# Kernel optimization log

Hardware: AMD Instinct MI355X
Metric: run time of the kernel (lower is better)

## Reference

```python
import jax, jax.numpy as jnp
import numpy as np

S_LEN, BATCH, HID, HEADS = 2048, 4, 1024, 16
HD = HID // HEADS


def setup_inputs() -> dict:
    key = jax.random.key(0)
    ks = jax.random.split(key, 6)

    def lin_w(k, out_dim, in_dim):
        return jax.random.normal(k, (out_dim, in_dim), jnp.float32) * (1.0 / np.sqrt(in_dim))

    return {
        "hidden_states": jax.random.normal(ks[0], (S_LEN, BATCH, HID), jnp.float32),
        "Wq": lin_w(ks[1], HID, HID), "bq": jnp.zeros((HID,), jnp.float32),
        "Wk": lin_w(ks[2], HID, HID), "bk": jnp.zeros((HID,), jnp.float32),
        "Wv": lin_w(ks[3], HID, HID), "bv": jnp.zeros((HID,), jnp.float32),
        "Wf": lin_w(ks[4], HEADS, HID), "bf": jnp.zeros((HEADS,), jnp.float32),
        "Wo": lin_w(ks[5], HID, HID), "bo": jnp.zeros((HID,), jnp.float32),
    }


def _forget_attention(hidden_states, Wq, bq, Wk, bk, Wv, bv, Wf, bf, Wo, bo):
    S, B, H = hidden_states.shape
    nh, hd = HEADS, HD

    def shape(x):
        return x.reshape(S, B, nh, hd)

    q = shape(hidden_states @ Wq.T + bq)
    k = shape(hidden_states @ Wk.T + bk)
    v = shape(hidden_states @ Wv.T + bv)

    # kernel_fn = elu(x) + 1
    phi_q = jax.nn.elu(q) + 1.0
    phi_k = jax.nn.elu(k) + 1.0

    f = jax.nn.sigmoid(hidden_states @ Wf.T + bf)  # [S, B, nh]

    # F_{t,j} = prod_{i=j+1}^{t} f_i  factorizes into the recurrence:
    #   S_t = f_t * S_{t-1} + phi_k_t (x) v_t ;  z_t = f_t * z_{t-1} + phi_k_t
    # out_t = (phi_q_t . S_t) / (phi_q_t . z_t + eps)
    def step(carry, xs):
        Sm, z = carry                      # [B,nh,hd,hd], [B,nh,hd]
        ft, pk, pq, vt = xs                # [B,nh], [B,nh,hd] x3
        fte = ft[..., None]
        Sm = fte[..., None] * Sm + pk[..., :, None] * vt[..., None, :]
        z = fte * z + pk
        num = jnp.einsum('bhd,bhde->bhe', pq, Sm)
        den = jnp.einsum('bhd,bhd->bh', pq, z)[..., None]
        return (Sm, z), num / (den + 1e-6)

    init = (jnp.zeros((B, nh, hd, hd), hidden_states.dtype),
            jnp.zeros((B, nh, hd), hidden_states.dtype))
    _, out = jax.lax.scan(step, init, (f, phi_k, phi_q, v))

    out = out.reshape(S, B, H) @ Wo.T + bo
    return out, f


def reference(hidden_states, Wq, bq, Wk, bk, Wv, bv, Wf, bf, Wo, bo):
    out, f = _forget_attention(hidden_states, Wq, bq, Wk, bk, Wv, bv, Wf, bf, Wo, bo)
    return (out, jnp.zeros_like(out), f)
```

## Files before the change

### kernel.cpp

```cpp
#include <hip/hip_runtime.h>
#include <hip/hip_bf16.h>
#include <math.h>

#define S_LEN 2048
#define BATCH 4
#define HID   1024
#define HEADS 16
#define HD    64
#define SB    (S_LEN*BATCH)
#define CHUNK 64
#define NCHUNK (S_LEN/CHUNK)
#define BH    (BATCH*HEADS)
#define NSTK  3200

typedef __bf16 bf16x8 __attribute__((ext_vector_type(8)));
typedef float  f32x4  __attribute__((ext_vector_type(4)));
typedef unsigned short ushort_t;
typedef unsigned short u16x8 __attribute__((ext_vector_type(8)));
typedef unsigned short u16x4 __attribute__((ext_vector_type(4)));

__device__ __forceinline__ unsigned short f2bf(float x) {
    union { float f; unsigned int u; } un; un.f = x;
    unsigned int u = un.u;
    unsigned int r = (u + 0x7FFFu + ((u >> 16) & 1u)) >> 16;
    return (unsigned short)r;
}
__device__ __forceinline__ float bf2f(unsigned short s) {
    union { unsigned int u; float f; } un; un.u = ((unsigned int)s) << 16;
    return un.f;
}

#define GLL16(src, dst) __builtin_amdgcn_global_load_lds( \
    (const __attribute__((address_space(1))) void*)(src), \
    (__attribute__((address_space(3))) void*)(dst), 16, 0, 0)

#define NXU (SB*HID/4)
#define NW1 (NSTK*HID/4)
#define NW2 (HID*HID/4)
#define NBU (NSTK/4)
#define NTOT (NXU+NW1+NW2+NBU)

__global__ __launch_bounds__(256) void prep_kernel(
    const float* __restrict__ X,  const float* __restrict__ Wq,
    const float* __restrict__ Wk, const float* __restrict__ Wv,
    const float* __restrict__ Wf, const float* __restrict__ Wo,
    const float* __restrict__ bq, const float* __restrict__ bk,
    const float* __restrict__ bv, const float* __restrict__ bf,
    ushort_t* __restrict__ Xb, ushort_t* __restrict__ Wstk,
    ushort_t* __restrict__ Wob, float* __restrict__ bstk)
{
    const int i = blockIdx.x * 256 + threadIdx.x;
    if (i < NXU) {
        float4 v = ((const float4*)X)[i];
        ushort4 o; o.x=f2bf(v.x); o.y=f2bf(v.y); o.z=f2bf(v.z); o.w=f2bf(v.w);
        ((ushort4*)Xb)[i] = o;
    } else if (i < NXU + NW1) {
        const int idx4 = (i - NXU) * 4;
        const int row = idx4 >> 10, col = idx4 & 1023;
        float4 v;
        if      (row < 1024) v = *(const float4*)(Wq + (size_t)row*HID + col);
        else if (row < 2048) v = *(const float4*)(Wk + (size_t)(row-1024)*HID + col);
        else if (row < 3072) v = *(const float4*)(Wv + (size_t)(row-2048)*HID + col);
        else if (row < 3088) v = *(const float4*)(Wf + (size_t)(row-3072)*HID + col);
        else                 v = make_float4(0.f,0.f,0.f,0.f);
        ushort4 o; o.x=f2bf(v.x); o.y=f2bf(v.y); o.z=f2bf(v.z); o.w=f2bf(v.w);
        *(ushort4*)(Wstk + idx4) = o;
    } else if (i < NXU + NW1 + NW2) {
        const int idx4 = (i - NXU - NW1) * 4;
        float4 v = *(const float4*)(Wo + idx4);
        ushort4 o; o.x=f2bf(v.x); o.y=f2bf(v.y); o.z=f2bf(v.z); o.w=f2bf(v.w);
        *(ushort4*)(Wob + idx4) = o;
    } else if (i < NTOT) {
        const int idx4 = (i - NXU - NW1 - NW2) * 4;
        #pragma unroll
        for (int t = 0; t < 4; ++t) {
            const int c = idx4 + t;
            float v;
            if      (c < 1024) v = bq[c];
            else if (c < 2048) v = bk[c-1024];
            else if (c < 3072) v = bv[c-2048];
            else if (c < 3088) v = bf[c-3072];
            else               v = 0.f;
            bstk[c] = v;
        }
    }
}

__global__ __launch_bounds__(256) void qkvf_gemm(
    const ushort_t* __restrict__ X, const ushort_t* __restrict__ W,
    const float* __restrict__ bias,
    ushort_t* __restrict__ Q, ushort_t* __restrict__ Kr,
    ushort_t* __restrict__ V,
    float* __restrict__ f_out, float* __restrict__ logf_out)
{
    __shared__ ushort_t As[128 * 32];
    __shared__ ushort_t Bs[128 * 32];

    const int tid  = threadIdx.x;
    const int wave = tid >> 6, lane = tid & 63;
    const int waveM = wave >> 1, waveN = wave & 1;

    const int lin = blockIdx.y * 64 + blockIdx.x;
    const int L   = (lin & 7) * 200 + (lin >> 3);
    const int rowBase = (L & 63) * 128;
    const int colBase = (L >> 6) * 128;
    const int K = HID;

    f32x4 acc[4][4];
    #pragma unroll
    for (int i = 0; i < 4; ++i)
        #pragma unroll
        for (int j = 0; j < 4; ++j)
            acc[i][j] = (f32x4){0.f, 0.f, 0.f, 0.f};

    const int srow = lane >> 2;
    const int scol = (lane & 3) * 8;

    const ushort_t* gA0 = X + (size_t)(rowBase + wave*16 + srow) * K + scol;
    const ushort_t* gB0 = W + (size_t)(colBase + wave*16 + srow) * K + scol;
    ushort_t* lA = As + (wave*16)*32;
    ushort_t* lB = Bs + (wave*16)*32;

    const int fr = lane & 15;
    const int fk = (lane >> 4) * 8;

    for (int k0 = 0; k0 < K; k0 += 32) {
        GLL16(gA0 + k0,                lA);
        GLL16(gA0 + (size_t)64*K + k0, lA + 64*32);
        GLL16(gB0 + k0,                lB);
        GLL16(gB0 + (size_t)64*K + k0, lB + 64*32);

        __syncthreads();

        bf16x8 a[4], b[4];
        #pragma unroll
        for (int i = 0; i < 4; ++i)
            a[i] = *(const bf16x8*)(As + (waveM*64 + i*16 + fr)*32 + fk);
        #pragma unroll
        for (int j = 0; j < 4; ++j)
            b[j] = *(const bf16x8*)(Bs + (waveN*64 + j*16 + fr)*32 + fk);

        #pragma unroll
        for (int i = 0; i < 4; ++i)
            #pragma unroll
            for (int j = 0; j < 4; ++j)
                acc[i][j] = __builtin_amdgcn_mfma_f32_16x16x32_bf16(
                    a[i], b[j], acc[i][j], 0, 0, 0);

        __syncthreads();
    }

    const int er = (lane >> 4) * 4;
    const int ec = lane & 15;
    #pragma unroll
    for (int i = 0; i < 4; ++i) {
        #pragma unroll
        for (int j = 0; j < 4; ++j) {
            const int r0 = rowBase + waveM*64 + i*16 + er;
            const int c0 = colBase + waveN*64 + j*16;
            if (c0 >= 3088) continue;
            const int c  = c0 + ec;
            const float bv = bias[c];
            #pragma unroll
            for (int k = 0; k < 4; ++k) {
                float v = acc[i][j][k] + bv;
                const int r = r0 + k;
                if (c0 < 1024) {
                    v = (v > 0.f) ? (v + 1.f) : __expf(v);
                    Q[(size_t)r * HID + c] = f2bf(v);
                } else if (c0 < 2048) {
                    v = (v > 0.f) ? (v + 1.f) : __expf(v);
                    Kr[(size_t)r * HID + (c - 1024)] = f2bf(v);
                } else if (c0 < 3072) {
                    V[(size_t)r * HID + (c - 2048)] = f2bf(v);
                } else {
                    const int n = c - 3072;
                    const float fv = 1.f / (1.f + __expf(-v));
                    f_out[(size_t)r * HEADS + n]    = fv;
                    logf_out[(size_t)r * HEADS + n] = -__logf(1.f + __expf(-v));
                }
            }
        }
    }
}

__global__ __launch_bounds__(256) void gemm_out(
    const ushort_t* __restrict__ X, const ushort_t* __restrict__ W,
    const float* __restrict__ bias, float* __restrict__ Y)
{
    __shared__ ushort_t As[128 * 32];
    __shared__ ushort_t Bs[128 * 32];

    const int tid  = threadIdx.x;
    const int wave = tid >> 6, lane = tid & 63;
    const int waveM = wave >> 1, waveN = wave & 1;

    const int lin = blockIdx.y * 64 + blockIdx.x;
    const int L   = (lin & 7) * 64 + (lin >> 3);
    const int rowBase = (L & 63) * 128;
    const int colBase = (L >> 6) * 128;
    const int K = HID, N = HID;

    f32x4 acc[4][4];
    #pragma unroll
    for (int i = 0; i < 4; ++i)
        #pragma unroll
        for (int j = 0; j < 4; ++j)
            acc[i][j] = (f32x4){0.f, 0.f, 0.f, 0.f};

    const int srow = lane >> 2;
    const int scol = (lane & 3) * 8;

    const ushort_t* gA0 = X + (size_t)(rowBase + wave*16 + srow) * K + scol;
    const ushort_t* gB0 = W + (size_t)(colBase + wave*16 + srow) * K + scol;
    ushort_t* lA = As + (wave*16)*32;
    ushort_t* lB = Bs + (wave*16)*32;

    const int fr = lane & 15;
    const int fk = (lane >> 4) * 8;

    for (int k0 = 0; k0 < K; k0 += 32) {
        GLL16(gA0 + k0,                lA);
        GLL16(gA0 + (size_t)64*K + k0, lA + 64*32);
        GLL16(gB0 + k0,                lB);
        GLL16(gB0 + (size_t)64*K + k0, lB + 64*32);

        __syncthreads();

        bf16x8 a[4], b[4];
        #pragma unroll
        for (int i = 0; i < 4; ++i)
            a[i] = *(const bf16x8*)(As + (waveM*64 + i*16 + fr)*32 + fk);
        #pragma unroll
        for (int j = 0; j < 4; ++j)
            b[j] = *(const bf16x8*)(Bs + (waveN*64 + j*16 + fr)*32 + fk);

        #pragma unroll
        for (int i = 0; i < 4; ++i)
            #pragma unroll
            for (int j = 0; j < 4; ++j)
                acc[i][j] = __builtin_amdgcn_mfma_f32_16x16x32_bf16(
                    a[i], b[j], acc[i][j], 0, 0, 0);

        __syncthreads();
    }

    const int er = (lane >> 4) * 4;
    const int ec = lane & 15;
    #pragma unroll
    for (int i = 0; i < 4; ++i) {
        #pragma unroll
        for (int j = 0; j < 4; ++j) {
            const int r0 = rowBase + waveM*64 + i*16 + er;
            const int c  = colBase + waveN*64 + j*16 + ec;
            const float bv = bias[c];
            #pragma unroll
            for (int k = 0; k < 4; ++k) {
                const size_t off = (size_t)(r0 + k) * N + c;
                Y[off] = acc[i][j][k] + bv;
            }
        }
    }
}

__global__ __launch_bounds__(256) void pass1_kernel(
    const ushort_t* __restrict__ Kp, const ushort_t* __restrict__ Vp,
    const float* __restrict__ logf,
    ushort_t* __restrict__ Schunk, float* __restrict__ zchunk,
    float* __restrict__ Dchunk)
{
    __shared__ __align__(16) char smem[18688];
    ushort_t* vsT = (ushort_t*)smem;
    ushort_t* kTd = (ushort_t*)(smem + 9216);
    float*    exd = (float*)(smem + 18432);

    const int chunk = blockIdx.x;
    const int bh = blockIdx.y;
    const int b = bh >> 4, h = bh & 15;
    const int tid = threadIdx.x;
    const int wv = tid >> 6, ln = tid & 63;
    const int fr = ln & 15, q4 = ln >> 4;
    const size_t slot = (size_t)bh * NCHUNK + chunk;

    u16x8 vreg[2], kreg[2];
    #pragma unroll
    for (int it = 0; it < 2; ++it) {
        const int u = it*256 + tid;
        const int j = u >> 3, d8 = (u & 7) * 8;
        const size_t base = (size_t)((chunk*64 + j)*BATCH + b)*HID + h*HD + d8;
        vreg[it] = *(const u16x8*)(Vp + base);
        kreg[it] = *(const u16x8*)(Kp + base);
    }
    if (tid < 64) {
        float v = logf[(size_t)((chunk*64 + tid)*BATCH + b) * HEADS + h];
        #pragma unroll
        for (int off = 1; off < 64; off <<= 1) {
            float n = __shfl_up(v, off);
            if (tid >= off) v += n;
        }
        const float tot = __shfl(v, 63);
        exd[tid] = __expf(tot - v);
        if (tid == 63) Dchunk[slot] = __expf(tot);
    }
    __syncthreads();

    #pragma unroll
    for (int it = 0; it < 2; ++it) {
        const int u = it*256 + tid;
        const int j = u >> 3, d8 = (u & 7) * 8;
        const float ex = exd[j];
        #pragma unroll
        for (int i = 0; i < 8; ++i) {
            vsT[(d8+i)*72 + j] = vreg[it][i];
            kTd[(d8+i)*72 + j] = f2bf(bf2f(kreg[it][i]) * ex);
        }
    }
    __syncthreads();

    f32x4 acc[4];
    #pragma unroll
    for (int nt = 0; nt < 4; ++nt) acc[nt] = (f32x4){0.f,0.f,0.f,0.f};
    #pragma unroll
    for (int k0 = 0; k0 < 64; k0 += 32) {
        bf16x8 av = *(const bf16x8*)(vsT + (wv*16 + fr)*72 + k0 + q4*8);
        #pragma unroll
        for (int nt = 0; nt < 4; ++nt) {
            bf16x8 bk = *(const bf16x8*)(kTd + (nt*16 + fr)*72 + k0 + q4*8);
            acc[nt] = __builtin_amdgcn_mfma_f32_16x16x32_bf16(av, bk, acc[nt], 0, 0, 0);
        }
    }

    if (wv == 0) {
        u16x8 onesu;
        #pragma unroll
        for (int i = 0; i < 8; ++i) onesu[i] = 0x3F80;
        const bf16x8 ones = *(const bf16x8*)&onesu;
        f32x4 zacc[4];
        #pragma unroll
        for (int nt = 0; nt < 4; ++nt) zacc[nt] = (f32x4){0.f,0.f,0.f,0.f};
        #pragma unroll
        for (int k0 = 0; k0 < 64; k0 += 32) {
            #pragma unroll
            for (int nt = 0; nt < 4; ++nt) {
                bf16x8 bk = *(const bf16x8*)(kTd + (nt*16 + fr)*72 + k0 + q4*8);
                zacc[nt] = __builtin_amdgcn_mfma_f32_16x16x32_bf16(ones, bk, zacc[nt], 0, 0, 0);
            }
        }
        if (q4 == 0) {
            #pragma unroll
            for (int nt = 0; nt < 4; ++nt)
                zchunk[slot*64 + nt*16 + fr] = zacc[nt][0];
        }
    }

    ushort_t* sp = Schunk + slot * 4096;
    #pragma unroll
    for (int nt = 0; nt < 4; ++nt) {
        #pragma unroll
        for (int r = 0; r < 4; ++r) {
            const int e = wv*16 + q4*4 + r;
            sp[e*64 + nt*16 + fr] = f2bf(acc[nt][r]);
        }
    }
}

__global__ __launch_bounds__(128) void pass2_kernel(
    ushort_t* __restrict__ Schunk, float* __restrict__ zchunk,
    const float* __restrict__ Dchunk)
{
    __shared__ float Ds[NCHUNK];
    const int bh  = blockIdx.x >> 3;
    const int sl  = blockIdx.x & 7;
    const int tid = threadIdx.x;

    if (tid < NCHUNK) Ds[tid] = Dchunk[bh * NCHUNK + tid];

    float Sprev[4] = {0.f, 0.f, 0.f, 0.f};
    float zprev = 0.f;

    const size_t base  = (size_t)bh * NCHUNK * 4096 + sl * 512 + tid * 4;
    const size_t zbase = (size_t)bh * NCHUNK * 64;
    const bool doZ = (sl == 0) && (tid < 64);

    u16x4 b0 = *(const u16x4*)(Schunk + base);
    u16x4 b1 = *(const u16x4*)(Schunk + base + 4096);
    float z0v = 0.f, z1v = 0.f;
    if (doZ) {
        z0v = zchunk[zbase + tid];
        z1v = zchunk[zbase + 64 + tid];
    }
    __syncthreads();

    for (int c = 0; c < NCHUNK; ++c) {
        const float D = Ds[c];
        ushort_t* sp = Schunk + base + (size_t)c * 4096;
        u16x4 wout;
        #pragma unroll
        for (int i = 0; i < 4; ++i) {
            wout[i] = f2bf(Sprev[i]);
            Sprev[i] = D * Sprev[i] + bf2f(b0[i]);
        }
        *(u16x4*)sp = wout;
        b0 = b1;
        if (doZ) {
            zchunk[zbase + (size_t)c * 64 + tid] = zprev;
            zprev = D * zprev + z0v;
            z0v = z1v;
        }
        if (c + 2 < NCHUNK) {
            b1 = *(const u16x4*)(Schunk + base + (size_t)(c+2)*4096);
            if (doZ) z1v = zchunk[zbase + (size_t)(c+2)*64 + tid];
        }
    }
}

__global__ __launch_bounds__(256) void pass3_kernel(
    const ushort_t* __restrict__ Qp, const ushort_t* __restrict__ Kp,
    const ushort_t* __restrict__ Vp, const float* __restrict__ logf,
    const ushort_t* __restrict__ S0, const float* __restrict__ z0,
    ushort_t* __restrict__ AO)
{
    __shared__ __align__(16) char smem[28928];
    ushort_t* qs  = (ushort_t*)smem;
    ushort_t* ks  = (ushort_t*)(smem + 9216);
    ushort_t* vsT = (ushort_t*)(smem + 9216);
    ushort_t* psA = (ushort_t*)(smem + 18432);
    float* cc  = (float*)(smem + 27648);
    float* exT = (float*)(smem + 27904);
    float* qz  = (float*)(smem + 28160);
    float* den = (float*)(smem + 28416);
    float* zz  = (float*)(smem + 28672);

    const int chunk = blockIdx.x;
    const int bh = blockIdx.y;
    const int b = bh >> 4, h = bh & 15;
    const int tid = threadIdx.x;
    const int wv = tid >> 6, ln = tid & 63;
    const int fr = ln & 15, q4 = ln >> 4;
    const size_t slot = (size_t)bh * NCHUNK + chunk;

    u16x8 vreg[2];
    #pragma unroll
    for (int it = 0; it < 2; ++it) {
        const int u = it*256 + tid;
        const int j = u >> 3, d8 = (u & 7) * 8;
        vreg[it] = *(const u16x8*)(Vp + (size_t)((chunk*64 + j)*BATCH + b)*HID + h*HD + d8);
    }

    if (tid < 64) {
        zz[tid] = z0[slot * 64 + tid];
        float v = logf[(size_t)((chunk*64 + tid)*BATCH + b) * HEADS + h];
        #pragma unroll
        for (int off = 1; off < 64; off <<= 1) {
            float n = __shfl_up(v, off);
            if (tid >= off) v += n;
        }
        cc[tid]  = v;
        exT[tid] = __expf(v);
    }
    #pragma unroll
    for (int it = 0; it < 2; ++it) {
        const int u = it*256 + tid;
        const int r = u >> 3, c8 = (u & 7) * 8;
        const size_t goff = (size_t)((chunk*64 + r)*BATCH + b) * HID + h*HD + c8;
        *(u16x8*)(qs + r*72 + c8) = *(const u16x8*)(Qp + goff);
        *(u16x8*)(ks + r*72 + c8) = *(const u16x8*)(Kp + goff);
    }
    __syncthreads();

    f32x4 pacc[4];
    #pragma unroll
    for (int nt = 0; nt < 4; ++nt) pacc[nt] = (f32x4){0.f,0.f,0.f,0.f};
    #pragma unroll
    for (int k0 = 0; k0 < 64; k0 += 32) {
        bf16x8 af = *(const bf16x8*)(qs + (wv*16 + fr)*72 + k0 + q4*8);
        #pragma unroll
        for (int nt = 0; nt < 4; ++nt) {
            bf16x8 bfr = *(const bf16x8*)(ks + (nt*16 + fr)*72 + k0 + q4*8);
            pacc[nt] = __builtin_amdgcn_mfma_f32_16x16x32_bf16(af, bfr, pacc[nt], 0, 0, 0);
        }
    }
    {
        const int t = wv*16 + fr;
        const int d0 = q4 * 16;
        float s = 0.f;
        #pragma unroll
        for (int i = 0; i < 16; ++i)
            s += bf2f(qs[t*72 + d0 + i]) * zz[d0 + i];
        s += __shfl_xor(s, 16);
        s += __shfl_xor(s, 32);
        if (q4 == 0) qz[t] = s;
    }
    __syncthreads();

    #pragma unroll
    for (int it = 0; it < 2; ++it) {
        const int u = it*256 + tid;
        const int j = u >> 3, d8 = (u & 7) * 8;
        #pragma unroll
        for (int i = 0; i < 8; ++i)
            vsT[(d8+i)*72 + j] = vreg[it][i];
    }
    {
        float rs[4] = {0.f, 0.f, 0.f, 0.f};
        float cct[4];
        #pragma unroll
        for (int r = 0; r < 4; ++r) cct[r] = cc[wv*16 + q4*4 + r];
        #pragma unroll
        for (int nt = 0; nt < 4; ++nt) {
            const int j = nt*16 + fr;
            const float ccj = cc[j];
            #pragma unroll
            for (int r = 0; r < 4; ++r) {
                const int t = wv*16 + q4*4 + r;
                float p = (j <= t) ? pacc[nt][r] * __expf(cct[r] - ccj) : 0.f;
                rs[r] += p;
                psA[t*72 + j] = f2bf(p);
            }
        }
        #pragma unroll
        for (int m = 1; m < 16; m <<= 1) {
            #pragma unroll
            for (int r = 0; r < 4; ++r) rs[r] += __shfl_xor(rs[r], m);
        }
        if (fr == 0) {
            #pragma unroll
            for (int r = 0; r < 4; ++r) {
                const int t = wv*16 + q4*4 + r;
                den[t] = rs[r] + exT[t] * qz[t] + 1e-6f;
            }
        }
    }
    __syncthreads();

    f32x4 oacc[4], oacc2[4];
    #pragma unroll
    for (int nt = 0; nt < 4; ++nt) {
        oacc[nt]  = (f32x4){0.f,0.f,0.f,0.f};
        oacc2[nt] = (f32x4){0.f,0.f,0.f,0.f};
    }
    const ushort_t* S0p = S0 + slot * 4096;
    #pragma unroll
    for (int k0 = 0; k0 < 64; k0 += 32) {
        const int k8 = k0 + q4*8;
        bf16x8 ap = *(const bf16x8*)(psA + (wv*16 + fr)*72 + k8);
        bf16x8 aq = *(const bf16x8*)(qs  + (wv*16 + fr)*72 + k8);
        #pragma unroll
        for (int nt = 0; nt < 4; ++nt) {
            bf16x8 bv = *(const bf16x8*)(vsT + (nt*16 + fr)*72 + k8);
            oacc[nt] = __builtin_amdgcn_mfma_f32_16x16x32_bf16(ap, bv, oacc[nt], 0, 0, 0);
            bf16x8 sb = *(const bf16x8*)(S0p + (nt*16 + fr)*64 + k8);
            oacc2[nt] = __builtin_amdgcn_mfma_f32_16x16x32_bf16(aq, sb, oacc2[nt], 0, 0, 0);
        }
    }
    #pragma unroll
    for (int nt = 0; nt < 4; ++nt) {
        const int e = nt*16 + fr;
        #pragma unroll
        for (int r = 0; r < 4; ++r) {
            const int t = wv*16 + q4*4 + r;
            const float v = (oacc[nt][r] + exT[t] * oacc2[nt][r]) / den[t];
            AO[(size_t)((chunk*64 + t)*BATCH + b) * HID + h*HD + e] = f2bf(v);
        }
    }
}

extern "C" void kernel_launch(void* const* d_in, const int* in_sizes, int n_in,
                              void* d_out, int out_size, void* d_ws, size_t ws_size,
                              hipStream_t stream) {
    const float* X  = (const float*)d_in[0];
    const float* Wq = (const float*)d_in[1];
    const float* bq = (const float*)d_in[2];
    const float* Wk = (const float*)d_in[3];
    const float* bk = (const float*)d_in[4];
    const float* Wv = (const float*)d_in[5];
    const float* bv = (const float*)d_in[6];
    const float* Wf = (const float*)d_in[7];
    const float* bf = (const float*)d_in[8];
    const float* Wo = (const float*)d_in[9];
    const float* bo = (const float*)d_in[10];

    float* out = (float*)d_out;
    const size_t OUT_SLOT = (size_t)SB * HID;

    char* ws = (char*)d_ws;
    ushort_t* wsXb   = (ushort_t*)ws;
    ushort_t* wsWstk = wsXb + (size_t)SB * HID;
    ushort_t* wsWob  = wsWstk + (size_t)NSTK * HID;
    ushort_t* wsQ    = wsWob + (size_t)HID * HID;
    ushort_t* wsK    = wsQ + (size_t)SB * HID;
    ushort_t* wsV    = wsK + (size_t)SB * HID;
    float* wsBstk = (float*)(wsV + (size_t)SB * HID);
    float* wsLogf = wsBstk + NSTK;
    ushort_t* wsS  = (ushort_t*)(wsLogf + (size_t)SB * HEADS);
    float* wsZ    = (float*)(wsS + (size_t)BH * NCHUNK * HD * HD);
    float* wsD    = wsZ + (size_t)BH * NCHUNK * HD;

    hipMemsetAsync(out + OUT_SLOT, 0, OUT_SLOT * sizeof(float), stream);

    prep_kernel<<<(NTOT + 255)/256, 256, 0, stream>>>(
        X, Wq, Wk, Wv, Wf, Wo, bq, bk, bv, bf,
        wsXb, wsWstk, wsWob, wsBstk);

    dim3 qgrid(64, 25);
    qkvf_gemm<<<qgrid, 256, 0, stream>>>(
        wsXb, wsWstk, wsBstk, wsQ, wsK, wsV,
        out + 2*OUT_SLOT, wsLogf);

    dim3 sgrid(NCHUNK, BH);
    pass1_kernel<<<sgrid, 256, 0, stream>>>(wsK, wsV, wsLogf, wsS, wsZ, wsD);
    pass2_kernel<<<BH*8, 128, 0, stream>>>(wsS, wsZ, wsD);
    pass3_kernel<<<sgrid, 256, 0, stream>>>(wsQ, wsK, wsV, wsLogf, wsS, wsZ, wsXb);

    dim3 ogrid(64, 8);
    gemm_out<<<ogrid, 256, 0, stream>>>(wsXb, wsWob, bo, out);
}
```

Before: 296.3 us.

## Swizzle transposed LDS tiles and simplify GEMM block mapping

Applies an XOR swizzle to the column index of the transposed V and decayed-K LDS tiles in the chunk passes, with matching swizzled reads for the MFMA operand loads, to reduce LDS bank conflicts. It also drops the XCD-aware block index remapping in the QKVF and output GEMMs in favour of a direct blockIdx-to-tile mapping. The simpler mapping may change L2 locality across chiplets.

```diff
diff --git a/kernel.cpp b/kernel.cpp
--- a/kernel.cpp
+++ b/kernel.cpp
@@ -29,6 +29,8 @@
     union { unsigned int u; float f; } un; un.u = ((unsigned int)s) << 16;
     return un.f;
 }
+
+#define JSW(row, j) ((j) ^ ((((row) >> 3) & 7) << 3))
 
 #define GLL16(src, dst) __builtin_amdgcn_global_load_lds( \
     (const __attribute__((address_space(1))) void*)(src), \
@@ -99,11 +101,8 @@
     const int tid  = threadIdx.x;
     const int wave = tid >> 6, lane = tid & 63;
     const int waveM = wave >> 1, waveN = wave & 1;
-
-    const int lin = blockIdx.y * 64 + blockIdx.x;
-    const int L   = (lin & 7) * 200 + (lin >> 3);
-    const int rowBase = (L & 63) * 128;
-    const int colBase = (L >> 6) * 128;
+    const int rowBase = blockIdx.x * 128;
+    const int colBase = blockIdx.y * 128;
     const int K = HID;
 
     f32x4 acc[4][4];
@@ -194,11 +193,8 @@
     const int tid  = threadIdx.x;
     const int wave = tid >> 6, lane = tid & 63;
     const int waveM = wave >> 1, waveN = wave & 1;
-
-    const int lin = blockIdx.y * 64 + blockIdx.x;
-    const int L   = (lin & 7) * 64 + (lin >> 3);
-    const int rowBase = (L & 63) * 128;
-    const int colBase = (L >> 6) * 128;
+    const int rowBase = blockIdx.x * 128;
+    const int colBase = blockIdx.y * 128;
     const int K = HID, N = HID;
 
     f32x4 acc[4][4];
@@ -308,11 +304,12 @@
     for (int it = 0; it < 2; ++it) {
         const int u = it*256 + tid;
         const int j = u >> 3, d8 = (u & 7) * 8;
+        const int js = j ^ ((u & 7) << 3);
         const float ex = exd[j];
         #pragma unroll
         for (int i = 0; i < 8; ++i) {
-            vsT[(d8+i)*72 + j] = vreg[it][i];
-            kTd[(d8+i)*72 + j] = f2bf(bf2f(kreg[it][i]) * ex);
+            vsT[(d8+i)*72 + js] = vreg[it][i];
+            kTd[(d8+i)*72 + js] = f2bf(bf2f(kreg[it][i]) * ex);
         }
     }
     __syncthreads();
@@ -322,10 +319,12 @@
     for (int nt = 0; nt < 4; ++nt) acc[nt] = (f32x4){0.f,0.f,0.f,0.f};
     #pragma unroll
     for (int k0 = 0; k0 < 64; k0 += 32) {
-        bf16x8 av = *(const bf16x8*)(vsT + (wv*16 + fr)*72 + k0 + q4*8);
+        const int rA = wv*16 + fr;
+        bf16x8 av = *(const bf16x8*)(vsT + rA*72 + JSW(rA, k0 + q4*8));
         #pragma unroll
         for (int nt = 0; nt < 4; ++nt) {
-            bf16x8 bk = *(const bf16x8*)(kTd + (nt*16 + fr)*72 + k0 + q4*8);
+            const int rB = nt*16 + fr;
+            bf16x8 bk = *(const bf16x8*)(kTd + rB*72 + JSW(rB, k0 + q4*8));
             acc[nt] = __builtin_amdgcn_mfma_f32_16x16x32_bf16(av, bk, acc[nt], 0, 0, 0);
         }
     }
@@ -342,7 +341,8 @@
         for (int k0 = 0; k0 < 64; k0 += 32) {
             #pragma unroll
             for (int nt = 0; nt < 4; ++nt) {
-                bf16x8 bk = *(const bf16x8*)(kTd + (nt*16 + fr)*72 + k0 + q4*8);
+                const int rB = nt*16 + fr;
+                bf16x8 bk = *(const bf16x8*)(kTd + rB*72 + JSW(rB, k0 + q4*8));
                 zacc[nt] = __builtin_amdgcn_mfma_f32_16x16x32_bf16(ones, bk, zacc[nt], 0, 0, 0);
             }
         }
@@ -497,9 +497,10 @@
     for (int it = 0; it < 2; ++it) {
         const int u = it*256 + tid;
         const int j = u >> 3, d8 = (u & 7) * 8;
+        const int js = j ^ ((u & 7) << 3);
         #pragma unroll
         for (int i = 0; i < 8; ++i)
-            vsT[(d8+i)*72 + j] = vreg[it][i];
+            vsT[(d8+i)*72 + js] = vreg[it][i];
     }
     {
         float rs[4] = {0.f, 0.f, 0.f, 0.f};
@@ -547,9 +548,10 @@
         bf16x8 aq = *(const bf16x8*)(qs  + (wv*16 + fr)*72 + k8);
         #pragma unroll
         for (int nt = 0; nt < 4; ++nt) {
-            bf16x8 bv = *(const bf16x8*)(vsT + (nt*16 + fr)*72 + k8);
+            const int rV = nt*16 + fr;
+            bf16x8 bv = *(const bf16x8*)(vsT + rV*72 + JSW(rV, k8));
             oacc[nt] = __builtin_amdgcn_mfma_f32_16x16x32_bf16(ap, bv, oacc[nt], 0, 0, 0);
-            bf16x8 sb = *(const bf16x8*)(S0p + (nt*16 + fr)*64 + k8);
+            bf16x8 sb = *(const bf16x8*)(S0p + rV*64 + k8);
             oacc2[nt] = __builtin_amdgcn_mfma_f32_16x16x32_bf16(aq, sb, oacc2[nt], 0, 0, 0);
         }
     }
@@ -602,7 +604,7 @@
         X, Wq, Wk, Wv, Wf, Wo, bq, bk, bv, bf,
         wsXb, wsWstk, wsWob, wsBstk);
 
-    dim3 qgrid(64, 25);
+    dim3 qgrid(SB/128, NSTK/128);
     qkvf_gemm<<<qgrid, 256, 0, stream>>>(
         wsXb, wsWstk, wsBstk, wsQ, wsK, wsV,
         out + 2*OUT_SLOT, wsLogf);
@@ -612,6 +614,6 @@
     pass2_kernel<<<BH*8, 128, 0, stream>>>(wsS, wsZ, wsD);
     pass3_kernel<<<sgrid, 256, 0, stream>>>(wsQ, wsK, wsV, wsLogf, wsS, wsZ, wsXb);
 
-    dim3 ogrid(64, 8);
+    dim3 ogrid(SB/128, HID/128);
     gemm_out<<<ogrid, 256, 0, stream>>>(wsXb, wsWob, bo, out);
 }
```

Result: faster. 284.3 us (-4.0%).
